# Performance work log

Measured on AMD Instinct MI355X. Metric: run time of the kernel, lower is better.

## Reference

```python
import jax, jax.numpy as jnp
from jax import lax
import numpy as np

WIN = 9
PAD = WIN // 2
DN = ('NCDHW', 'OIDHW', 'NCDHW')


def box_sum(x):
    """9x9x9 all-ones box sum (same padding), computed separably per axis.
    Matches the original dense depthwise conv3d with a ones kernel exactly in math."""
    C = x.shape[1]
    for axis in range(3):  # spatial axes D, H, W
        kshape = [1, 1, 1]
        kshape[axis] = WIN
        kernel = jnp.ones((C, 1, *kshape), dtype=x.dtype)
        padding = [(PAD, PAD) if i == axis else (0, 0) for i in range(3)]
        x = lax.conv_general_dilated(
            x, kernel, window_strides=(1, 1, 1), padding=padding,
            dimension_numbers=DN, feature_group_count=C)
    return x


def setup_inputs() -> dict:
    key = jax.random.key(0)
    k1, k2 = jax.random.split(key)
    shape = (2, 1, 160, 192, 160)
    y_true = jax.random.uniform(k1, shape, dtype=jnp.float32)
    y_pred = jax.random.uniform(k2, shape, dtype=jnp.float32)
    return {"y_true": y_true, "y_pred": y_pred}


def reference(y_true, y_pred):
    Ii, Ji = y_true, y_pred
    win_size = jnp.asarray(WIN ** 3, dtype=Ii.dtype)

    I_sum = box_sum(Ii)
    J_sum = box_sum(Ji)
    I2_sum = box_sum(Ii * Ii)
    J2_sum = box_sum(Ji * Ji)
    IJ_sum = box_sum(Ii * Ji)

    u_I = I_sum / win_size
    u_J = J_sum / win_size

    cross = IJ_sum - u_I * J_sum
    I_var = jnp.maximum(I2_sum - u_I * I_sum, 1e-05)
    J_var = jnp.maximum(J2_sum - u_J * J_sum, 1e-05)

    cc = cross * cross / (I_var * J_var + 1e-05)
    return -jnp.sum(cc)
```

## Files before the change

kernel.cpp:

```cpp
#include <hip/hip_runtime.h>
#include <hip/hip_fp16.h>

#define ND 2
#define DD 160
#define HH 192
#define WW 160
#define HW (HH * WW)
#define DHW (DD * HH * WW)

constexpr int TW  = 32;
constexpr int TH  = 32;
constexpr int HLO = TH + 8;
constexpr int FCH = 20;
constexpr int NCH = DD / FCH;
constexpr int NSL = FCH + 8;
constexpr int NR  = NSL / 2;

struct alignas(8) h4 { __half2 lo, hi; };

__device__ __forceinline__ void slide4(const float x[12], float S[4]) {
    float f = ((x[0] + x[1]) + (x[2] + x[3]))
            + ((x[4] + x[5]) + (x[6] + x[7])) + x[8];
    S[0] = f;
    f += x[9]  - x[0]; S[1] = f;
    f += x[10] - x[1]; S[2] = f;
    f += x[11] - x[2]; S[3] = f;
}

#define RUPD(RG, RS, NH, N4, P0, P1, P2, P3, P4)            \
    P0 += __low2float((NH).lo)  - __low2float((RG).lo);     \
    P1 += __high2float((NH).lo) - __high2float((RG).lo);    \
    P2 += __low2float((NH).hi)  - __low2float((RG).hi);     \
    P3 += __high2float((NH).hi) - __high2float((RG).hi);    \
    P4 += __half2float(N4)      - __half2float(RS);         \
    RG = (NH); RS = (N4);

__global__ __launch_bounds__(512)
void ncc_fused8(const float* __restrict__ I, const float* __restrict__ J,
                float* __restrict__ outp)
{
    __shared__ float  sraw[2][3328];
    __shared__ float4 sws[2][HLO][TW + 1];
    __shared__ float  sw4[2][HLO][TW + 1];
    __shared__ float  wred[8];

    const int tid = threadIdx.x;
    const int w0  = blockIdx.x * TW;
    const int h0  = blockIdx.y * TH;
    const int z   = blockIdx.z;
    const int n   = z >> 3;
    const int d0  = (z & 7) * FCH;

    const int hp = (tid >> 5) * 2;
    const int ow = tid & 31;
    const int ha = h0 + hp, hb = ha + 1, wg = w0 + ow;
    const float cWv  = (float)(min(wg + 4, WW - 1) - max(wg - 4, 0) + 1);
    const float cHWa = cWv * (float)(min(ha + 4, HH - 1) - max(ha - 4, 0) + 1);
    const float cHWb = cWv * (float)(min(hb + 4, HH - 1) - max(hb - 4, 0) + 1);

    const bool c1I  = tid < 400;
    const int  cr1  = c1I ? tid : tid - 400;
    const int  cro1 = cr1 / 10, cwc1 = cr1 - cro1 * 10;
    const int  gh1  = h0 + cro1 - 4, gw1 = w0 - 4 + cwc1 * 4;
    const bool sp1  = gh1 >= 0 && gh1 < HH && gw1 >= 0 && gw1 < WW;
    const float* f1 = c1I ? I : J;
    const int  o1   = sp1 ? (gh1 * WW + gw1) : 0;
    const int  cr2  = 112 + tid;
    const int  cro2 = cr2 / 10, cwc2 = cr2 - cro2 * 10;
    const int  gh2  = h0 + cro2 - 4, gw2 = w0 - 4 + cwc2 * 4;
    const bool sp2  = gh2 >= 0 && gh2 < HH && gw2 >= 0 && gw2 < WW;
    const int  o2   = sp2 ? (gh2 * WW + gw2) : 0;
    const int  base1 = (tid & ~63) * 4;
    const int  base2 = (512 + (tid & ~63)) * 4;

    auto stage = [&](int p, int dd) {
        const bool dok = (dd >= 0) && (dd < DD);
        const size_t sb = (size_t)(n * DD + dd) * HW;
        const float* s1 = (dok && sp1) ? (f1 + sb + o1) : f1;
        __builtin_amdgcn_global_load_lds(
            (const __attribute__((address_space(1))) void*)s1,
            (__attribute__((address_space(3))) void*)&sraw[p][base1], 16, 0, 0);
        if (tid < 288) {
            const float* s2 = (dok && sp2) ? (J + sb + o2) : J;
            __builtin_amdgcn_global_load_lds(
                (const __attribute__((address_space(1))) void*)s2,
                (__attribute__((address_space(3))) void*)&sraw[p][base2], 16, 0, 0);
        }
    };

    h4 gA0, gA1, gA2, gA3, gA4, gA5, gA6, gA7, gA8;
    h4 gB0, gB1, gB2, gB3, gB4, gB5, gB6, gB7, gB8;
    __half sA0, sA1, sA2, sA3, sA4, sA5, sA6, sA7, sA8;
    __half sB0, sB1, sB2, sB3, sB4, sB5, sB6, sB7, sB8;
    {
        h4 zz; zz.lo = __floats2half2_rn(0.f, 0.f); zz.hi = zz.lo;
        const __half z1 = __float2half(0.f);
        gA0=gA1=gA2=gA3=gA4=gA5=gA6=gA7=gA8=zz;
        gB0=gB1=gB2=gB3=gB4=gB5=gB6=gB7=gB8=zz;
        sA0=sA1=sA2=sA3=sA4=sA5=sA6=sA7=sA8=z1;
        sB0=sB1=sB2=sB3=sB4=sB5=sB6=sB7=sB8=z1;
    }
    float rA0=0.f, rA1=0.f, rA2=0.f, rA3=0.f, rA4=0.f;
    float rB0=0.f, rB1=0.f, rB2=0.f, rB3=0.f, rB4=0.f;
    float acc = 0.f;
    const float inv = 1.0f / 729.0f;

    stage(0, d0 - 4 + 0);
    stage(1, d0 - 4 + 1);
    __syncthreads();

    #pragma unroll 1
    for (int g = 0; g < 2; ++g) {
        #pragma unroll
        for (int r = 0; r < 9; ++r) {
            const int rr = g * 9 + r;
            if (rr < NR) {
                const int s0  = 2 * rr;
                const int dd0 = d0 - 4 + s0;
                #pragma unroll
                for (int jb = 0; jb < 2; ++jb) {
                    const int job = tid + jb * 512;
                    if (job < 8 * HLO * 2) {
                        const int sl   = job >= 320;
                        const int rj   = job - sl * 320;
                        const int arow = rj >> 3;
                        const int awg  = rj & 7;
                        const int agh  = h0 + arow - 4;
                        const bool ahok = (agh >= 0) && (agh < HH);
                        const int agws = w0 + awg * 4 - 4;
                        const int dd   = dd0 + sl;
                        const bool dok = (dd >= 0) && (dd < DD);
                        float a[12], b[12];
                        const int fi = arow * 40 + awg * 4;
                        #pragma unroll
                        for (int c = 0; c < 3; ++c) {
                            const int gw = agws + 4 * c;
                            float4 va = *(const float4*)&sraw[sl][fi + 4 * c];
                            float4 vb = *(const float4*)&sraw[sl][1600 + fi + 4 * c];
                            if (dok && ahok && gw >= 0 && gw < WW) {
                                va.x -= 0.5f; va.y -= 0.5f; va.z -= 0.5f; va.w -= 0.5f;
                                vb.x -= 0.5f; vb.y -= 0.5f; vb.z -= 0.5f; vb.w -= 0.5f;
                            } else {
                                va = make_float4(0.f, 0.f, 0.f, 0.f); vb = va;
                            }
                            *(float4*)&a[4 * c] = va;
                            *(float4*)&b[4 * c] = vb;
                        }
                        if (dok) {
                            float S0[4], S1[4], S2[4], S3[4], S4[4], f[12];
                            slide4(a, S0);
                            slide4(b, S1);
                            #pragma unroll
                            for (int i = 0; i < 12; ++i) f[i] = a[i] * a[i];
                            slide4(f, S2);
                            #pragma unroll
                            for (int i = 0; i < 12; ++i) f[i] = b[i] * b[i];
                            slide4(f, S3);
                            #pragma unroll
                            for (int i = 0; i < 12; ++i) f[i] = a[i] * b[i];
                            slide4(f, S4);
                            #pragma unroll
                            for (int t = 0; t < 4; ++t) {
                                sws[sl][arow][awg * 4 + t] =
                                    make_float4(S0[t], S1[t], S2[t], S3[t]);
                                sw4[sl][arow][awg * 4 + t] = S4[t];
                            }
                        }
                    }
                }
                __syncthreads();
                if (rr + 1 < NR) {
                    stage(0, dd0 + 2);
                    stage(1, dd0 + 3);
                }
                #pragma unroll
                for (int half = 0; half < 2; ++half) {
                    const int s   = s0 + half;
                    const int ddx = dd0 + half;
                    float t0=0.f,t1=0.f,t2=0.f,t3=0.f,t4=0.f;
                    float u0=0.f,u1=0.f,u2=0.f,u3=0.f,u4=0.f;
                    if (ddx >= 0 && ddx < DD) {
                        const float4 r0 = sws[half][hp][ow];
                        const float  r04 = sw4[half][hp][ow];
                        t0 = r0.x; t1 = r0.y; t2 = r0.z; t3 = r0.w; t4 = r04;
                        #pragma unroll
                        for (int q = 1; q < 9; ++q) {
                            const float4 v = sws[half][hp + q][ow];
                            t0 += v.x; t1 += v.y; t2 += v.z; t3 += v.w;
                            t4 += sw4[half][hp + q][ow];
                        }
                        const float4 v9 = sws[half][hp + 9][ow];
                        u0 = t0 + v9.x - r0.x;
                        u1 = t1 + v9.y - r0.y;
                        u2 = t2 + v9.z - r0.z;
                        u3 = t3 + v9.w - r0.w;
                        u4 = t4 + sw4[half][hp + 9][ow] - r04;
                    }
                    h4 nhA, nhB;
                    nhA.lo = __floats2half2_rn(t0, t1);
                    nhA.hi = __floats2half2_rn(t2, t3);
                    nhB.lo = __floats2half2_rn(u0, u1);
                    nhB.hi = __floats2half2_rn(u2, u3);
                    const __half n4A = __float2half(t4);
                    const __half n4B = __float2half(u4);
                    const int jj = (2 * r + half) % 9;
                    if      (jj == 0) { RUPD(gA0,sA0,nhA,n4A,rA0,rA1,rA2,rA3,rA4)
                                        RUPD(gB0,sB0,nhB,n4B,rB0,rB1,rB2,rB3,rB4) }
                    else if (jj == 1) { RUPD(gA1,sA1,nhA,n4A,rA0,rA1,rA2,rA3,rA4)
                                        RUPD(gB1,sB1,nhB,n4B,rB0,rB1,rB2,rB3,rB4) }
                    else if (jj == 2) { RUPD(gA2,sA2,nhA,n4A,rA0,rA1,rA2,rA3,rA4)
                                        RUPD(gB2,sB2,nhB,n4B,rB0,rB1,rB2,rB3,rB4) }
                    else if (jj == 3) { RUPD(gA3,sA3,nhA,n4A,rA0,rA1,rA2,rA3,rA4)
                                        RUPD(gB3,sB3,nhB,n4B,rB0,rB1,rB2,rB3,rB4) }
                    else if (jj == 4) { RUPD(gA4,sA4,nhA,n4A,rA0,rA1,rA2,rA3,rA4)
                                        RUPD(gB4,sB4,nhB,n4B,rB0,rB1,rB2,rB3,rB4) }
                    else if (jj == 5) { RUPD(gA5,sA5,nhA,n4A,rA0,rA1,rA2,rA3,rA4)
                                        RUPD(gB5,sB5,nhB,n4B,rB0,rB1,rB2,rB3,rB4) }
                    else if (jj == 6) { RUPD(gA6,sA6,nhA,n4A,rA0,rA1,rA2,rA3,rA4)
                                        RUPD(gB6,sB6,nhB,n4B,rB0,rB1,rB2,rB3,rB4) }
                    else if (jj == 7) { RUPD(gA7,sA7,nhA,n4A,rA0,rA1,rA2,rA3,rA4)
                                        RUPD(gB7,sB7,nhB,n4B,rB0,rB1,rB2,rB3,rB4) }
                    else              { RUPD(gA8,sA8,nhA,n4A,rA0,rA1,rA2,rA3,rA4)
                                        RUPD(gB8,sB8,nhB,n4B,rB0,rB1,rB2,rB3,rB4) }
                    if (s >= 8) {
                        const int d = d0 + s - 8;
                        const float cD = (float)(min(d + 4, DD - 1) - max(d - 4, 0) + 1);
                        {
                            const float cnt = cHWa * cD;
                            const float Is = rA0 + 0.5f * cnt;
                            const float Js = rA1 + 0.5f * cnt;
                            const float I2 = rA2 + rA0 + 0.25f * cnt;
                            const float J2 = rA3 + rA1 + 0.25f * cnt;
                            const float IJ = rA4 + 0.5f * (rA0 + rA1) + 0.25f * cnt;
                            const float uI = Is * inv, uJ = Js * inv;
                            const float cross = IJ - uI * Js;
                            const float Iv = fmaxf(I2 - uI * Is, 1e-5f);
                            const float Jv = fmaxf(J2 - uJ * Js, 1e-5f);
                            acc += cross * cross / (Iv * Jv + 1e-5f);
                        }
                        {
                            const float cnt = cHWb * cD;
                            const float Is = rB0 + 0.5f * cnt;
                            const float Js = rB1 + 0.5f * cnt;
                            const float I2 = rB2 + rB0 + 0.25f * cnt;
                            const float J2 = rB3 + rB1 + 0.25f * cnt;
                            const float IJ = rB4 + 0.5f * (rB0 + rB1) + 0.25f * cnt;
                            const float uI = Is * inv, uJ = Js * inv;
                            const float cross = IJ - uI * Js;
                            const float Iv = fmaxf(I2 - uI * Is, 1e-5f);
                            const float Jv = fmaxf(J2 - uJ * Js, 1e-5f);
                            acc += cross * cross / (Iv * Jv + 1e-5f);
                        }
                    }
                }
                __syncthreads();
            }
        }
    }

    #pragma unroll
    for (int off = 32; off > 0; off >>= 1)
        acc += __shfl_down(acc, off, 64);
    const int lane = tid & 63, wid = tid >> 6;
    if (lane == 0) wred[wid] = acc;
    __syncthreads();
    if (tid == 0) {
        float ssum = 0.f;
        #pragma unroll
        for (int i = 0; i < 8; ++i) ssum += wred[i];
        atomicAdd(outp, -ssum);
    }
}

extern "C" void kernel_launch(void* const* d_in, const int* in_sizes, int n_in,
                              void* d_out, int out_size, void* d_ws, size_t ws_size,
                              hipStream_t stream)
{
    const float* I = (const float*)d_in[0];
    const float* J = (const float*)d_in[1];
    float* out = (float*)d_out;

    hipMemsetAsync(out, 0, sizeof(float), stream);
    dim3 grid(WW / TW, HH / TH, ND * NCH);
    ncc_fused8<<<grid, 512, 0, stream>>>(I, J, out);
}
```

Measured before the change: 163.3 us.

## Widen W-pass jobs to 8 outputs and pack IJ row-pairs as float2

The W-direction sliding-sum stage now gives each of 320 threads 8 outputs instead of 4, so 320 jobs fit in a single pass rather than two per-thread iterations. This cuts redundant halo loads and adds. The IJ product sum is stored as float2 row pairs, so the H-direction pass reads 5 float2 values instead of 10 scalars. Launch bounds now request 4 waves per SIMD, which constrains register allocation. The wider per-thread job raises register pressure and leaves 192 threads idle during this stage.

```diff
diff --git a/kernel.cpp b/kernel.cpp
--- a/kernel.cpp
+++ b/kernel.cpp
@@ -18,7 +18,7 @@
 
 struct alignas(8) h4 { __half2 lo, hi; };
 
-__device__ __forceinline__ void slide4(const float x[12], float S[4]) {
+__device__ __forceinline__ void slide4(const float* x, float* S) {
     float f = ((x[0] + x[1]) + (x[2] + x[3]))
             + ((x[4] + x[5]) + (x[6] + x[7])) + x[8];
     S[0] = f;
@@ -35,13 +35,13 @@
     P4 += __half2float(N4)      - __half2float(RS);         \
     RG = (NH); RS = (N4);
 
-__global__ __launch_bounds__(512)
-void ncc_fused8(const float* __restrict__ I, const float* __restrict__ J,
+__global__ __launch_bounds__(512, 4)
+void ncc_fused9(const float* __restrict__ I, const float* __restrict__ J,
                 float* __restrict__ outp)
 {
     __shared__ float  sraw[2][3328];
-    __shared__ float4 sws[2][HLO][TW + 1];
-    __shared__ float  sw4[2][HLO][TW + 1];
+    __shared__ float4 sws4[2][HLO][TW + 1];
+    __shared__ float2 swIJ[2][HLO / 2][TW + 1];
     __shared__ float  wred[8];
 
     const int tid = threadIdx.x;
@@ -51,8 +51,19 @@
     const int n   = z >> 3;
     const int d0  = (z & 7) * FCH;
 
-    const int hp = (tid >> 5) * 2;
-    const int ow = tid & 31;
+    const bool ajob = (tid < 320);
+    const int  sl   = tid >= 160;
+    const int  rj   = tid - sl * 160;
+    const int  arow = rj >> 2;
+    const int  awg  = rj & 3;
+    const int  agh  = h0 + arow - 4;
+    const bool ahok = (agh >= 0) && (agh < HH);
+    const int  agws = w0 + awg * 8 - 4;
+    const int  fi   = arow * 40 + awg * 8;
+
+    const int hp  = (tid >> 5) * 2;
+    const int hpp = hp >> 1;
+    const int ow  = tid & 31;
     const int ha = h0 + hp, hb = ha + 1, wg = w0 + ow;
     const float cWv  = (float)(min(wg + 4, WW - 1) - max(wg - 4, 0) + 1);
     const float cHWa = cWv * (float)(min(ha + 4, HH - 1) - max(ha - 4, 0) + 1);
@@ -117,55 +128,45 @@
             if (rr < NR) {
                 const int s0  = 2 * rr;
                 const int dd0 = d0 - 4 + s0;
-                #pragma unroll
-                for (int jb = 0; jb < 2; ++jb) {
-                    const int job = tid + jb * 512;
-                    if (job < 8 * HLO * 2) {
-                        const int sl   = job >= 320;
-                        const int rj   = job - sl * 320;
-                        const int arow = rj >> 3;
-                        const int awg  = rj & 7;
-                        const int agh  = h0 + arow - 4;
-                        const bool ahok = (agh >= 0) && (agh < HH);
-                        const int agws = w0 + awg * 4 - 4;
-                        const int dd   = dd0 + sl;
-                        const bool dok = (dd >= 0) && (dd < DD);
-                        float a[12], b[12];
-                        const int fi = arow * 40 + awg * 4;
-                        #pragma unroll
-                        for (int c = 0; c < 3; ++c) {
-                            const int gw = agws + 4 * c;
-                            float4 va = *(const float4*)&sraw[sl][fi + 4 * c];
-                            float4 vb = *(const float4*)&sraw[sl][1600 + fi + 4 * c];
-                            if (dok && ahok && gw >= 0 && gw < WW) {
-                                va.x -= 0.5f; va.y -= 0.5f; va.z -= 0.5f; va.w -= 0.5f;
-                                vb.x -= 0.5f; vb.y -= 0.5f; vb.z -= 0.5f; vb.w -= 0.5f;
-                            } else {
-                                va = make_float4(0.f, 0.f, 0.f, 0.f); vb = va;
-                            }
-                            *(float4*)&a[4 * c] = va;
-                            *(float4*)&b[4 * c] = vb;
-                        }
-                        if (dok) {
-                            float S0[4], S1[4], S2[4], S3[4], S4[4], f[12];
-                            slide4(a, S0);
-                            slide4(b, S1);
-                            #pragma unroll
-                            for (int i = 0; i < 12; ++i) f[i] = a[i] * a[i];
-                            slide4(f, S2);
-                            #pragma unroll
-                            for (int i = 0; i < 12; ++i) f[i] = b[i] * b[i];
-                            slide4(f, S3);
-                            #pragma unroll
-                            for (int i = 0; i < 12; ++i) f[i] = a[i] * b[i];
-                            slide4(f, S4);
-                            #pragma unroll
-                            for (int t = 0; t < 4; ++t) {
-                                sws[sl][arow][awg * 4 + t] =
-                                    make_float4(S0[t], S1[t], S2[t], S3[t]);
-                                sw4[sl][arow][awg * 4 + t] = S4[t];
-                            }
-                        }
+                if (ajob) {
+                    const int dd   = dd0 + sl;
+                    const bool dok = (dd >= 0) && (dd < DD);
+                    float a[16], b[16];
+                    #pragma unroll
+                    for (int c = 0; c < 4; ++c) {
+                        const int gw = agws + 4 * c;
+                        float4 va = *(const float4*)&sraw[sl][fi + 4 * c];
+                        float4 vb = *(const float4*)&sraw[sl][1600 + fi + 4 * c];
+                        if (dok && ahok && gw >= 0 && gw < WW) {
+                            va.x -= 0.5f; va.y -= 0.5f; va.z -= 0.5f; va.w -= 0.5f;
+                            vb.x -= 0.5f; vb.y -= 0.5f; vb.z -= 0.5f; vb.w -= 0.5f;
+                        } else {
+                            va = make_float4(0.f, 0.f, 0.f, 0.f); vb = va;
+                        }
+                        *(float4*)&a[4 * c] = va;
+                        *(float4*)&b[4 * c] = vb;
+                    }
+                    if (dok) {
+                        float f[16], S[8];
+                        #pragma unroll
+                        for (int i = 0; i < 16; ++i) f[i] = a[i] * b[i];
+                        slide4(f, S); slide4(f + 4, S + 4);
+                        #pragma unroll
+                        for (int t = 0; t < 8; ++t)
+                            ((float*)&swIJ[sl][arow >> 1][awg * 8 + t])[arow & 1] = S[t];
+                        float SI[8], SJ[8], SII[8], SJJ[8];
+                        slide4(a, SI); slide4(a + 4, SI + 4);
+                        slide4(b, SJ); slide4(b + 4, SJ + 4);
+                        #pragma unroll
+                        for (int i = 0; i < 16; ++i) f[i] = a[i] * a[i];
+                        slide4(f, SII); slide4(f + 4, SII + 4);
+                        #pragma unroll
+                        for (int i = 0; i < 16; ++i) f[i] = b[i] * b[i];
+                        slide4(f, SJJ); slide4(f + 4, SJJ + 4);
+                        #pragma unroll
+                        for (int t = 0; t < 8; ++t)
+                            sws4[sl][arow][awg * 8 + t] =
+                                make_float4(SI[t], SJ[t], SII[t], SJJ[t]);
                     }
                 }
                 __syncthreads();
@@ -180,21 +181,26 @@
                     float t0=0.f,t1=0.f,t2=0.f,t3=0.f,t4=0.f;
                     float u0=0.f,u1=0.f,u2=0.f,u3=0.f,u4=0.f;
                     if (ddx >= 0 && ddx < DD) {
-                        const float4 r0 = sws[half][hp][ow];
-                        const float  r04 = sw4[half][hp][ow];
-                        t0 = r0.x; t1 = r0.y; t2 = r0.z; t3 = r0.w; t4 = r04;
+                        const float4 r0 = sws4[half][hp][ow];
+                        t0 = r0.x; t1 = r0.y; t2 = r0.z; t3 = r0.w;
                         #pragma unroll
                         for (int q = 1; q < 9; ++q) {
-                            const float4 v = sws[half][hp + q][ow];
+                            const float4 v = sws4[half][hp + q][ow];
                             t0 += v.x; t1 += v.y; t2 += v.z; t3 += v.w;
-                            t4 += sw4[half][hp + q][ow];
-                        }
-                        const float4 v9 = sws[half][hp + 9][ow];
+                        }
+                        const float4 v9 = sws4[half][hp + 9][ow];
                         u0 = t0 + v9.x - r0.x;
                         u1 = t1 + v9.y - r0.y;
                         u2 = t2 + v9.z - r0.z;
                         u3 = t3 + v9.w - r0.w;
-                        u4 = t4 + sw4[half][hp + 9][ow] - r04;
+                        const float2 ij0 = swIJ[half][hpp + 0][ow];
+                        const float2 ij1 = swIJ[half][hpp + 1][ow];
+                        const float2 ij2 = swIJ[half][hpp + 2][ow];
+                        const float2 ij3 = swIJ[half][hpp + 3][ow];
+                        const float2 ij4 = swIJ[half][hpp + 4][ow];
+                        t4 = ((ij0.x + ij0.y) + (ij1.x + ij1.y))
+                           + ((ij2.x + ij2.y) + (ij3.x + ij3.y)) + ij4.x;
+                        u4 = t4 + ij4.y - ij0.x;
                     }
                     h4 nhA, nhB;
                     nhA.lo = __floats2half2_rn(t0, t1);
@@ -282,5 +288,5 @@
 
     hipMemsetAsync(out, 0, sizeof(float), stream);
     dim3 grid(WW / TW, HH / TH, ND * NCH);
-    ncc_fused8<<<grid, 512, 0, stream>>>(I, J, out);
+    ncc_fused9<<<grid, 512, 0, stream>>>(I, J, out);
 }
```

Measured after the change: 212.1 us. 29.9% more time.
